# Optimization experiments

Measured on AMD Instinct MI355X. Metric: run time of the kernel, lower is better.

## Reference

```python
import jax, jax.numpy as jnp
import numpy as np

B, N, M = 8, 4096, 2048
IN_DIM, D, CTX_DIM = 512, 512, 768


def setup_inputs() -> dict:
    key = jax.random.key(0)
    k_h, k_hr, k_c, k_a, k_k, k_v, k_o = jax.random.split(key, 7)
    s = 0.02  # init scale for weights
    return {
        "h": jax.random.normal(k_h, (B, N, IN_DIM), dtype=jnp.float32),
        "h_retrieved": jax.random.normal(k_hr, (B, M, CTX_DIM), dtype=jnp.float32),
        # torch nn.Linear convention: weight is [out_features, in_features]
        "W_cond": jax.random.normal(k_c, (IN_DIM, CTX_DIM), dtype=jnp.float32) * s,
        "W_attn": jax.random.normal(k_a, (D, IN_DIM), dtype=jnp.float32) * s,
        "W_k": jax.random.normal(k_k, (D, IN_DIM), dtype=jnp.float32) * s,
        "W_v": jax.random.normal(k_v, (D, IN_DIM), dtype=jnp.float32) * s,
        "W_out": jax.random.normal(k_o, (IN_DIM, D), dtype=jnp.float32) * s,
    }


def reference(h, h_retrieved, W_cond, W_attn, W_k, W_v, W_out):
    # cond_flag is True since context_dim != in_dim
    hr = h_retrieved @ W_cond.T                      # [B, M, in_dim]
    attn = jax.nn.softmax(h @ W_attn.T, axis=-1)     # [B, N, d], softmax over channel dim
    kv_in = jnp.concatenate([h, hr], axis=1)         # [B, N+M, in_dim]
    k = kv_in @ W_k.T                                # [B, N+M, d]
    v = kv_in @ W_v.T                                # [B, N+M, d]
    f = jnp.einsum('bnd,bne->bde', k, v)             # K^T V: [B, d, d]
    h_aug = jnp.einsum('bnd,bde->bne', attn, f)      # [B, N, d]
    return h + h_aug @ W_out.T                       # [B, N, in_dim]
```

## Files before the change

### kernel.cpp

```cpp
#include <hip/hip_runtime.h>
#include <hip/hip_bf16.h>


typedef unsigned short u16;
typedef __bf16 bf16x8 __attribute__((ext_vector_type(8)));
typedef float  f32x4  __attribute__((ext_vector_type(4)));
typedef float  f32v4  __attribute__((ext_vector_type(4)));
typedef u16    u16v4  __attribute__((ext_vector_type(4)));
typedef u16    u16v8  __attribute__((ext_vector_type(8)));

__device__ __forceinline__ u16 f2bf(float f) {
  unsigned u = __builtin_bit_cast(unsigned, f);
  u = u + 0x7FFFu + ((u >> 16) & 1u);
  return (u16)(u >> 16);
}
__device__ __forceinline__ float bf2f(u16 s) {
  return __builtin_bit_cast(float, (unsigned)s << 16);
}

__global__ __launch_bounds__(256) void cvt_dual(const float* __restrict__ src,
                                                u16* __restrict__ dstN,
                                                u16* __restrict__ dstT,
                                                long src_bs, long dstT_bs) {
  __shared__ u16 tile[64][72];
  long bz = blockIdx.z;
  const float* S = src + bz * src_bs;
  u16* DN = dstN + bz * src_bs;
  u16* DT = dstT + bz * dstT_bs;
  int r0 = blockIdx.x * 64;
  int c0 = blockIdx.y * 64;
  int t  = threadIdx.x;
  int tr = t >> 2;
  int tc = (t & 3) * 16;
  const float* sp = &S[(long)(r0 + tr) * 512 + c0 + tc];
#pragma unroll
  for (int q = 0; q < 2; ++q) {
    f32v4 a = *(const f32v4*)(sp + q * 8);
    f32v4 b = *(const f32v4*)(sp + q * 8 + 4);
    u16v8 o;
    o[0] = f2bf(a[0]); o[1] = f2bf(a[1]); o[2] = f2bf(a[2]); o[3] = f2bf(a[3]);
    o[4] = f2bf(b[0]); o[5] = f2bf(b[1]); o[6] = f2bf(b[2]); o[7] = f2bf(b[3]);
    *(u16v8*)&DN[(long)(r0 + tr) * 512 + c0 + tc + q * 8] = o;
    *(u16v8*)&tile[tr][tc + q * 8] = o;
  }
  __syncthreads();
  int tr2 = t >> 3;
  int tc2 = (t & 7) * 8;
#pragma unroll
  for (int it = 0; it < 2; ++it) {
    int cr = it * 32 + tr2;
    u16v8 o;
#pragma unroll
    for (int j = 0; j < 8; ++j) o[j] = tile[tc2 + j][cr];
    *(u16v8*)&DT[(long)(c0 + cr) * 6144 + r0 + tc2] = o;
  }
}

__global__ __launch_bounds__(256) void prep_weights(
    const float* __restrict__ Wc, const float* __restrict__ Wa,
    const float* __restrict__ Wk, const float* __restrict__ Wv,
    const float* __restrict__ Wo,
    u16* __restrict__ wc, u16* __restrict__ wa, u16* __restrict__ wk,
    u16* __restrict__ wv, u16* __restrict__ wvT, u16* __restrict__ wo) {
  __shared__ u16 tile[64][72];
  int bx = blockIdx.x;
  int t = threadIdx.x;
  if (bx < 576) {
    const float* src; u16* dst; long base;
    if (bx < 192)      { src = Wc; dst = wc; base = (long)bx * 2048; }
    else if (bx < 320) { src = Wa; dst = wa; base = (long)(bx - 192) * 2048; }
    else if (bx < 448) { src = Wk; dst = wk; base = (long)(bx - 320) * 2048; }
    else               { src = Wo; dst = wo; base = (long)(bx - 448) * 2048; }
    long i = base + (long)t * 8;
    f32v4 a = *(const f32v4*)(src + i);
    f32v4 b = *(const f32v4*)(src + i + 4);
    u16v8 o;
    o[0] = f2bf(a[0]); o[1] = f2bf(a[1]); o[2] = f2bf(a[2]); o[3] = f2bf(a[3]);
    o[4] = f2bf(b[0]); o[5] = f2bf(b[1]); o[6] = f2bf(b[2]); o[7] = f2bf(b[3]);
    *(u16v8*)(dst + i) = o;
  } else {
    int b2 = bx - 576;
    int r0 = (b2 >> 3) * 64, c0 = (b2 & 7) * 64;
    int tr = t >> 2, tc = (t & 3) * 16;
    const float* sp = &Wv[(long)(r0 + tr) * 512 + c0 + tc];
#pragma unroll
    for (int q = 0; q < 2; ++q) {
      f32v4 a = *(const f32v4*)(sp + q * 8);
      f32v4 b = *(const f32v4*)(sp + q * 8 + 4);
      u16v8 o;
      o[0] = f2bf(a[0]); o[1] = f2bf(a[1]); o[2] = f2bf(a[2]); o[3] = f2bf(a[3]);
      o[4] = f2bf(b[0]); o[5] = f2bf(b[1]); o[6] = f2bf(b[2]); o[7] = f2bf(b[3]);
      *(u16v8*)&wv[(long)(r0 + tr) * 512 + c0 + tc + q * 8] = o;
      *(u16v8*)&tile[tr][tc + q * 8] = o;
    }
    __syncthreads();
    int tr2 = t >> 3, tc2 = (t & 7) * 8;
#pragma unroll
    for (int it = 0; it < 2; ++it) {
      int cr = it * 32 + tr2;
      u16v8 o;
#pragma unroll
      for (int j = 0; j < 8; ++j) o[j] = tile[tc2 + j][cr];
      *(u16v8*)&wvT[(long)(c0 + cr) * 512 + r0 + tc2] = o;
    }
  }
}

__global__ __launch_bounds__(256) void reduce8_bf16(const u16* __restrict__ parts,
                                                    u16* __restrict__ out) {
  long i = (((long)blockIdx.x * 256) + threadIdx.x) * 8;
  long b = i >> 18;
  long r = i & 262143;
  const u16* p = parts + b * 2097152 + r;
  float acc[8] = {};
#pragma unroll
  for (int s = 0; s < 8; ++s) {
    u16v8 v = *(const u16v8*)(p + (long)s * 262144);
#pragma unroll
    for (int j = 0; j < 8; ++j) acc[j] += bf2f(v[j]);
  }
  u16v8 o;
#pragma unroll
  for (int j = 0; j < 8; ++j) o[j] = f2bf(acc[j]);
  *(u16v8*)(out + i) = o;
}

template <int MODE>
__global__ __launch_bounds__(256) void gemm_nt(
    const u16* __restrict__ A, const u16* __restrict__ B, void* __restrict__ Cout,
    const float* __restrict__ Res, int K, int lda, int ldb, int ldc,
    long sA, long sB, long sC, long sS, long sRes, int kslices) {
  __shared__ __align__(16) char smem_c[32768];
  u16* As = (u16*)smem_c;
  u16* Bs = (u16*)(smem_c + 16384);

  int gx = gridDim.x, gy = gridDim.y;
  int nwg = gx * gy * (int)gridDim.z;
  int flat = blockIdx.x + gx * (blockIdx.y + gy * blockIdx.z);
  if ((nwg & 7) == 0) { int q = nwg >> 3; flat = (flat & 7) * q + (flat >> 3); }
  int bx = flat % gx; int tmp = flat / gx; int by = tmp % gy; int z = tmp / gy;

  int b = z / kslices;
  int s = z - b * kslices;
  const u16* Ag = A + (long)b * sA + (long)s * K;
  const u16* Bg = B + (long)b * sB + (long)s * K;

  long m0 = (long)bx * 128;
  long n0 = (long)by * 128;

  int tid  = threadIdx.x;
  int lane = tid & 63;
  int wid  = tid >> 6;
  int wm = wid >> 1, wn = wid & 1;

  int srow = wid * 8 + (lane >> 3);
  int scol = (lane & 7) * 8;

  f32x4 acc[4][4] = {};

  for (int k0 = 0; k0 < K; k0 += 64) {
#pragma unroll
    for (int c = 0; c < 4; ++c) {
      int row = c * 32 + srow;
      __builtin_amdgcn_global_load_lds(
          (const __attribute__((address_space(1))) void*)(Ag + (m0 + row) * lda + k0 + scol),
          (__attribute__((address_space(3))) void*)(As + (c * 32 + wid * 8) * 64),
          16, 0, 0);
    }
#pragma unroll
    for (int c = 0; c < 4; ++c) {
      int row = c * 32 + srow;
      __builtin_amdgcn_global_load_lds(
          (const __attribute__((address_space(1))) void*)(Bg + (n0 + row) * ldb + k0 + scol),
          (__attribute__((address_space(3))) void*)(Bs + (c * 32 + wid * 8) * 64),
          16, 0, 0);
    }
    __syncthreads();
#pragma unroll
    for (int kk = 0; kk < 2; ++kk) {
      int kofs = kk * 32 + (lane >> 4) * 8;
      bf16x8 af[4], bfr[4];
#pragma unroll
      for (int i = 0; i < 4; ++i) {
        af[i]  = *(const bf16x8*)&As[(wm * 64 + i * 16 + (lane & 15)) * 64 + kofs];
        bfr[i] = *(const bf16x8*)&Bs[(wn * 64 + i * 16 + (lane & 15)) * 64 + kofs];
      }
#pragma unroll
      for (int i = 0; i < 4; ++i)
#pragma unroll
        for (int j = 0; j < 4; ++j)
          acc[i][j] = __builtin_amdgcn_mfma_f32_16x16x32_bf16(af[i], bfr[j], acc[i][j], 0, 0, 0);
    }
    __syncthreads();
  }

  float* ep = (float*)(smem_c + wid * 4608);
  long cb  = (long)b * sC + (long)s * sS;
  int row0 = (int)m0 + wm * 64;
  int colb = (int)n0 + wn * 64;
  int lq = lane >> 4;
  int lr = lane & 15;

#pragma unroll
  for (int i = 0; i < 4; ++i) {
#pragma unroll
    for (int j = 0; j < 4; ++j)
#pragma unroll
      for (int r = 0; r < 4; ++r)
        ep[(lq * 4 + r) * 72 + lr + j * 16] = acc[i][j][r];
#pragma unroll
    for (int p = 0; p < 4; ++p) {
      int rl = p * 4 + lq;
      f32x4 v = *(f32x4*)&ep[rl * 72 + lr * 4];
      long off = (long)(row0 + i * 16 + rl) * ldc + colb + lr * 4;
      if (MODE == 0) {
        u16v4 o;
#pragma unroll
        for (int t = 0; t < 4; ++t) o[t] = f2bf(v[t]);
        *(u16v4*)((u16*)Cout + cb + off) = o;
      } else {
        const float* R = Res + (long)b * sRes;
        f32v4 rv = *(const f32v4*)&R[off];
        f32v4 ov;
#pragma unroll
        for (int t = 0; t < 4; ++t) ov[t] = v[t] + rv[t];
        *(f32v4*)((float*)Cout + cb + off) = ov;
      }
    }
  }
}

template <int MODE, bool AF32>
__global__ __launch_bounds__(256) void gemm64(
    const void* __restrict__ Ap, const u16* __restrict__ B, void* __restrict__ Cout,
    const float* __restrict__ Res, int K, int lda, int ldb, int ldc,
    long sA, long sB, long sC, long sRes) {
  __shared__ __align__(16) char smem_c[24576];
  u16* As = (u16*)smem_c;
  u16* Bs = (u16*)(smem_c + 8192);

  int gx = gridDim.x, gy = gridDim.y;
  int nwg = gx * gy * (int)gridDim.z;
  int flat = blockIdx.x + gx * (blockIdx.y + gy * blockIdx.z);
  if ((nwg & 7) == 0) { int q = nwg >> 3; flat = (flat & 7) * q + (flat >> 3); }
  int bx = flat % gx; int tmp = flat / gx; int by = tmp % gy; int b = tmp / gy;

  long n0 = (long)bx * 128;
  long m0 = (long)by * 64;
  const u16* Ag = (const u16*)Ap + (long)b * sA;
  const float* Af = (const float*)Ap + (long)b * sA;
  const u16* Bg = B + (long)b * sB;

  int tid  = threadIdx.x;
  int lane = tid & 63;
  int wid  = tid >> 6;
  int wm = wid >> 1, wn = wid & 1;

  int srow = wid * 8 + (lane >> 3);
  int scol = (lane & 7) * 8;

  f32x4 acc[2][4] = {};

  for (int k0 = 0; k0 < K; k0 += 64) {
    if constexpr (AF32) {
      int arow = tid >> 2;
      int acol = (tid & 3) * 16;
      const float* sp = Af + (m0 + arow) * (long)lda + k0 + acol;
      f32v4 x0 = *(const f32v4*)sp;
      f32v4 x1 = *(const f32v4*)(sp + 4);
      f32v4 x2 = *(const f32v4*)(sp + 8);
      f32v4 x3 = *(const f32v4*)(sp + 12);
      u16v8 o0, o1;
      o0[0] = f2bf(x0[0]); o0[1] = f2bf(x0[1]); o0[2] = f2bf(x0[2]); o0[3] = f2bf(x0[3]);
      o0[4] = f2bf(x1[0]); o0[5] = f2bf(x1[1]); o0[6] = f2bf(x1[2]); o0[7] = f2bf(x1[3]);
      o1[0] = f2bf(x2[0]); o1[1] = f2bf(x2[1]); o1[2] = f2bf(x2[2]); o1[3] = f2bf(x2[3]);
      o1[4] = f2bf(x3[0]); o1[5] = f2bf(x3[1]); o1[6] = f2bf(x3[2]); o1[7] = f2bf(x3[3]);
      *(u16v8*)&As[arow * 64 + acol] = o0;
      *(u16v8*)&As[arow * 64 + acol + 8] = o1;
    } else {
#pragma unroll
      for (int c = 0; c < 2; ++c) {
        int row = c * 32 + srow;
        __builtin_amdgcn_global_load_lds(
            (const __attribute__((address_space(1))) void*)(Ag + (m0 + row) * lda + k0 + scol),
            (__attribute__((address_space(3))) void*)(As + (c * 32 + wid * 8) * 64),
            16, 0, 0);
      }
    }
#pragma unroll
    for (int c = 0; c < 4; ++c) {
      int row = c * 32 + srow;
      __builtin_amdgcn_global_load_lds(
          (const __attribute__((address_space(1))) void*)(Bg + (n0 + row) * ldb + k0 + scol),
          (__attribute__((address_space(3))) void*)(Bs + (c * 32 + wid * 8) * 64),
          16, 0, 0);
    }
    __syncthreads();
#pragma unroll
    for (int kk = 0; kk < 2; ++kk) {
      int kofs = kk * 32 + (lane >> 4) * 8;
      bf16x8 af[2], bfr[4];
#pragma unroll
      for (int i = 0; i < 2; ++i)
        af[i]  = *(const bf16x8*)&As[(wm * 32 + i * 16 + (lane & 15)) * 64 + kofs];
#pragma unroll
      for (int j = 0; j < 4; ++j)
        bfr[j] = *(const bf16x8*)&Bs[(wn * 64 + j * 16 + (lane & 15)) * 64 + kofs];
#pragma unroll
      for (int i = 0; i < 2; ++i)
#pragma unroll
        for (int j = 0; j < 4; ++j)
          acc[i][j] = __builtin_amdgcn_mfma_f32_16x16x32_bf16(af[i], bfr[j], acc[i][j], 0, 0, 0);
    }
    __syncthreads();
  }

  int lq = lane >> 4;
  int lr = lane & 15;

  if (MODE == 0 || MODE == 1) {
    float* ep = (float*)(smem_c + wid * 4608);
    long cb  = (long)b * sC;
    int row0 = (int)m0 + wm * 32;
    int colb = (int)n0 + wn * 64;
#pragma unroll
    for (int i = 0; i < 2; ++i) {
#pragma unroll
      for (int j = 0; j < 4; ++j)
#pragma unroll
        for (int r = 0; r < 4; ++r)
          ep[(lq * 4 + r) * 72 + lr + j * 16] = acc[i][j][r];
#pragma unroll
      for (int p = 0; p < 4; ++p) {
        int rl = p * 4 + lq;
        f32x4 v = *(f32x4*)&ep[rl * 72 + lr * 4];
        long off = (long)(row0 + i * 16 + rl) * ldc + colb + lr * 4;
        if (MODE == 0) {
          u16v4 o;
#pragma unroll
          for (int t = 0; t < 4; ++t) o[t] = f2bf(v[t]);
          *(u16v4*)((u16*)Cout + cb + off) = o;
        } else {
          const float* R = Res + (long)b * sRes;
          f32v4 rv = *(const f32v4*)&R[off];
          f32v4 ov;
#pragma unroll
          for (int t = 0; t < 4; ++t) ov[t] = v[t] + rv[t];
          *(f32v4*)((float*)Cout + cb + off) = ov;
        }
      }
    }
  } else {
    u16* tT = (u16*)smem_c;
#pragma unroll
    for (int i = 0; i < 2; ++i)
#pragma unroll
      for (int j = 0; j < 4; ++j)
#pragma unroll
        for (int r = 0; r < 4; ++r)
          tT[(wn * 64 + j * 16 + lr) * 72 + wm * 32 + i * 16 + lq * 4 + r] = f2bf(acc[i][j][r]);
    __syncthreads();
    long cb = (long)b * sC;
    int ct  = tid >> 1;
    int seg = (tid & 1) * 32;
    u16* dst = (u16*)Cout + cb + (long)(n0 + ct) * ldc + m0 + seg;
    const u16* srcl = &tT[ct * 72 + seg];
#pragma unroll
    for (int q = 0; q < 4; ++q)
      *(u16v8*)(dst + q * 8) = *(const u16v8*)(srcl + q * 8);
  }
}

__global__ __launch_bounds__(256, 2) void gemm_sm(
    const u16* __restrict__ A,
    const u16* __restrict__ Bw,
    u16* __restrict__ C) {
  __shared__ __align__(16) char smem[73728];
  u16* As = (u16*)smem;
  u16* Bs = (u16*)(smem + 8192);

  int nwg = gridDim.x;
  int flat = blockIdx.x;
  if ((nwg & 7) == 0) { int q = nwg >> 3; flat = (flat & 7) * q + (flat >> 3); }
  long m0 = (long)flat * 64;

  int tid = threadIdx.x;
  int lane = tid & 63;
  int wid = tid >> 6;

  int srow = wid * 8 + (lane >> 3);
  int scol = (lane & 7) * 8;

  f32x4 acc[4][8] = {};

  for (int k0 = 0; k0 < 512; k0 += 64) {
#pragma unroll
    for (int c = 0; c < 2; ++c) {
      int row = c * 32 + srow;
      __builtin_amdgcn_global_load_lds(
          (const __attribute__((address_space(1))) void*)(A + (m0 + row) * 512 + k0 + scol),
          (__attribute__((address_space(3))) void*)(As + (c * 32 + wid * 8) * 64),
          16, 0, 0);
    }
#pragma unroll
    for (int c = 0; c < 16; ++c) {
      int row = c * 32 + srow;
      __builtin_amdgcn_global_load_lds(
          (const __attribute__((address_space(1))) void*)(Bw + (long)row * 512 + k0 + scol),
          (__attribute__((address_space(3))) void*)(Bs + (c * 32 + wid * 8) * 64),
          16, 0, 0);
    }
    __syncthreads();
#pragma unroll
    for (int kk = 0; kk < 2; ++kk) {
      int kofs = kk * 32 + (lane >> 4) * 8;
      bf16x8 af[4], bfr[8];
#pragma unroll
      for (int i = 0; i < 4; ++i)
        af[i] = *(const bf16x8*)&As[(i * 16 + (lane & 15)) * 64 + kofs];
#pragma unroll
      for (int j = 0; j < 8; ++j)
        bfr[j] = *(const bf16x8*)&Bs[(wid * 128 + j * 16 + (lane & 15)) * 64 + kofs];
#pragma unroll
      for (int i = 0; i < 4; ++i)
#pragma unroll
        for (int j = 0; j < 8; ++j)
          acc[i][j] = __builtin_amdgcn_mfma_f32_16x16x32_bf16(af[i], bfr[j], acc[i][j], 0, 0, 0);
    }
    __syncthreads();
  }

  int lq = lane >> 4, lr = lane & 15;
  float* sm = (float*)smem;
  float* ss = (float*)(smem + 1024);

#pragma unroll
  for (int i = 0; i < 4; ++i)
#pragma unroll
    for (int r = 0; r < 4; ++r) {
      float m = acc[i][0][r];
#pragma unroll
      for (int j = 1; j < 8; ++j) m = fmaxf(m, acc[i][j][r]);
#pragma unroll
      for (int o = 1; o < 16; o <<= 1) m = fmaxf(m, __shfl_xor(m, o, 16));
      if (lr == 0) sm[(i * 16 + lq * 4 + r) * 4 + wid] = m;
    }
  __syncthreads();
  float rinv[4][4];
#pragma unroll
  for (int i = 0; i < 4; ++i)
#pragma unroll
    for (int r = 0; r < 4; ++r) {
      f32v4 g4 = *(const f32v4*)&sm[(i * 16 + lq * 4 + r) * 4];
      float gm = fmaxf(fmaxf(g4[0], g4[1]), fmaxf(g4[2], g4[3]));
      float s = 0.f;
#pragma unroll
      for (int j = 0; j < 8; ++j) {
        float e = __expf(acc[i][j][r] - gm);
        acc[i][j][r] = e;
        s += e;
      }
#pragma unroll
      for (int o = 1; o < 16; o <<= 1) s += __shfl_xor(s, o, 16);
      if (lr == 0) ss[(i * 16 + lq * 4 + r) * 4 + wid] = s;
    }
  __syncthreads();
#pragma unroll
  for (int i = 0; i < 4; ++i)
#pragma unroll
    for (int r = 0; r < 4; ++r) {
      f32v4 g4 = *(const f32v4*)&ss[(i * 16 + lq * 4 + r) * 4];
      rinv[i][r] = 1.0f / (g4[0] + g4[1] + g4[2] + g4[3]);
    }
  __syncthreads();

  float* ep = (float*)(smem + wid * 4608);
#pragma unroll
  for (int i = 0; i < 4; ++i) {
#pragma unroll
    for (int jh = 0; jh < 2; ++jh) {
#pragma unroll
      for (int j = 0; j < 4; ++j)
#pragma unroll
        for (int r = 0; r < 4; ++r)
          ep[(lq * 4 + r) * 72 + lr + j * 16] = acc[i][jh * 4 + j][r] * rinv[i][r];
#pragma unroll
      for (int p = 0; p < 4; ++p) {
        int rl = p * 4 + lq;
        f32x4 v = *(f32x4*)&ep[rl * 72 + lr * 4];
        u16v4 o;
#pragma unroll
        for (int t = 0; t < 4; ++t) o[t] = f2bf(v[t]);
        *(u16v4*)&C[(m0 + i * 16 + rl) * 512 + wid * 128 + jh * 64 + lr * 4] = o;
      }
    }
  }
}

extern "C" void kernel_launch(void* const* d_in, const int* in_sizes, int n_in,
                              void* d_out, int out_size, void* d_ws, size_t ws_size,
                              hipStream_t stream) {
  (void)in_sizes; (void)n_in; (void)out_size; (void)ws_size;
  const float* h    = (const float*)d_in[0];
  const float* hret = (const float*)d_in[1];
  const float* Wc   = (const float*)d_in[2];
  const float* Wa   = (const float*)d_in[3];
  const float* Wk   = (const float*)d_in[4];
  const float* Wv   = (const float*)d_in[5];
  const float* Wo   = (const float*)d_in[6];
  float* out = (float*)d_out;
  char*  ws  = (char*)d_ws;

  constexpr long MB = 1024 * 1024;
  u16*   w_cond = (u16*)(ws + 0);
  u16*   w_attn = (u16*)(ws + 786432);
  u16*   w_k    = (u16*)(ws + 1310720);
  u16*   w_v    = (u16*)(ws + 1835008);
  u16*   w_out  = (u16*)(ws + 2359296);
  u16*   w_vT   = (u16*)(ws + 2883584);
  u16*   h_bf   = (u16*)(ws + 4 * MB);
  u16*   gparts = (u16*)(ws + 4 * MB);
  u16*   attn   = (u16*)(ws + 36 * MB);
  u16*   g_bf   = (u16*)(ws + 68 * MB);
  u16*   u_mat  = (u16*)(ws + 72 * MB);
  u16*   v1     = (u16*)(ws + 73 * MB);
  u16*   f2t    = (u16*)(ws + 77 * MB);
  u16*   xt     = (u16*)(ws + 84 * MB);

  cvt_dual<<<dim3(64, 8, 8), 256, 0, stream>>>(h, h_bf, xt, 2097152L, 3145728L);
  prep_weights<<<640, 256, 0, stream>>>(Wc, Wa, Wk, Wv, Wo,
      w_cond, w_attn, w_k, w_v, w_vT, w_out);

  gemm64<3, true><<<dim3(4, 32, 8), 256, 0, stream>>>(hret, w_cond, xt + 4096, nullptr,
      768, 768, 768, 6144, 1572864L, 0, 3145728L, 0);

  gemm_sm<<<512, 256, 0, stream>>>(h_bf, w_attn, attn);

  gemm_nt<0><<<dim3(4, 4, 64), 256, 0, stream>>>(xt, xt, gparts, nullptr,
      768, 6144, 6144, 512, 3145728L, 3145728L, 2097152L, 262144L, 0, 8);
  reduce8_bf16<<<1024, 256, 0, stream>>>(gparts, g_bf);

  gemm64<0, false><<<dim3(4, 8, 1), 256, 0, stream>>>(w_out, w_vT, u_mat, nullptr,
      512, 512, 512, 512, 0, 0, 0, 0);
  gemm64<0, false><<<dim3(4, 8, 8), 256, 0, stream>>>(u_mat, g_bf, v1, nullptr,
      512, 512, 512, 512, 0, 262144L, 262144L, 0);
  gemm64<0, false><<<dim3(4, 8, 8), 256, 0, stream>>>(v1, w_k, f2t, nullptr,
      512, 512, 512, 512, 262144L, 0, 262144L, 0);

  gemm64<1, false><<<dim3(4, 64, 8), 256, 0, stream>>>(attn, f2t, out, h,
      512, 512, 512, 512, 2097152L, 262144L, 2097152L, 2097152L);
}
```

Before: 226.5 us.

## Double-buffer LDS tiles in both GEMM kernels to overlap loads with MFMA

Both GEMM kernels now use two LDS buffers per operand and issue the next K-tile's global-to-LDS loads (or fp32 register loads followed by bf16 conversion for the AF32 path) before running the MFMAs on the current tile. This drops one __syncthreads per iteration and is meant to hide global memory latency behind compute. In exchange, LDS use doubles (64KB and 48KB per block), which can lower occupancy, and register pressure rises on the AF32 path. Correctness depends on the s_waitcnt the compiler emits for global_load_lds before the single barrier.

Result: faster. 217.4 us (-4.0%).

```diff
diff --git a/kernel.cpp b/kernel.cpp
--- a/kernel.cpp
+++ b/kernel.cpp
@@ -130,9 +130,7 @@
     const u16* __restrict__ A, const u16* __restrict__ B, void* __restrict__ Cout,
     const float* __restrict__ Res, int K, int lda, int ldb, int ldc,
     long sA, long sB, long sC, long sS, long sRes, int kslices) {
-  __shared__ __align__(16) char smem_c[32768];
-  u16* As = (u16*)smem_c;
-  u16* Bs = (u16*)(smem_c + 16384);
+  __shared__ __align__(16) char smem_c[65536];
 
   int gx = gridDim.x, gy = gridDim.y;
   int nwg = gx * gy * (int)gridDim.z;
@@ -156,34 +154,51 @@
   int srow = wid * 8 + (lane >> 3);
   int scol = (lane & 7) * 8;
 
-  f32x4 acc[4][4] = {};
-
-  for (int k0 = 0; k0 < K; k0 += 64) {
+  auto stageA = [&](u16* Asd, int k0) {
 #pragma unroll
     for (int c = 0; c < 4; ++c) {
       int row = c * 32 + srow;
       __builtin_amdgcn_global_load_lds(
           (const __attribute__((address_space(1))) void*)(Ag + (m0 + row) * lda + k0 + scol),
-          (__attribute__((address_space(3))) void*)(As + (c * 32 + wid * 8) * 64),
+          (__attribute__((address_space(3))) void*)(Asd + (c * 32 + wid * 8) * 64),
           16, 0, 0);
     }
+  };
+  auto stageB = [&](u16* Bsd, int k0) {
 #pragma unroll
     for (int c = 0; c < 4; ++c) {
       int row = c * 32 + srow;
       __builtin_amdgcn_global_load_lds(
           (const __attribute__((address_space(1))) void*)(Bg + (n0 + row) * ldb + k0 + scol),
-          (__attribute__((address_space(3))) void*)(Bs + (c * 32 + wid * 8) * 64),
+          (__attribute__((address_space(3))) void*)(Bsd + (c * 32 + wid * 8) * 64),
           16, 0, 0);
     }
-    __syncthreads();
+  };
+
+  f32x4 acc[4][4] = {};
+  int nk = K >> 6;
+
+  stageA((u16*)smem_c, 0);
+  stageB((u16*)(smem_c + 32768), 0);
+  __syncthreads();
+
+  for (int t = 0; t < nk; ++t) {
+    u16* Asc = (u16*)(smem_c + (t & 1) * 16384);
+    u16* Bsc = (u16*)(smem_c + 32768 + (t & 1) * 16384);
+    if (t + 1 < nk) {
+      u16* Asn = (u16*)(smem_c + ((t + 1) & 1) * 16384);
+      u16* Bsn = (u16*)(smem_c + 32768 + ((t + 1) & 1) * 16384);
+      stageA(Asn, (t + 1) * 64);
+      stageB(Bsn, (t + 1) * 64);
+    }
 #pragma unroll
     for (int kk = 0; kk < 2; ++kk) {
       int kofs = kk * 32 + (lane >> 4) * 8;
       bf16x8 af[4], bfr[4];
 #pragma unroll
       for (int i = 0; i < 4; ++i) {
-        af[i]  = *(const bf16x8*)&As[(wm * 64 + i * 16 + (lane & 15)) * 64 + kofs];
-        bfr[i] = *(const bf16x8*)&Bs[(wn * 64 + i * 16 + (lane & 15)) * 64 + kofs];
+        af[i]  = *(const bf16x8*)&Asc[(wm * 64 + i * 16 + (lane & 15)) * 64 + kofs];
+        bfr[i] = *(const bf16x8*)&Bsc[(wn * 64 + i * 16 + (lane & 15)) * 64 + kofs];
       }
 #pragma unroll
       for (int i = 0; i < 4; ++i)
@@ -216,14 +231,14 @@
       if (MODE == 0) {
         u16v4 o;
 #pragma unroll
-        for (int t = 0; t < 4; ++t) o[t] = f2bf(v[t]);
+        for (int t2 = 0; t2 < 4; ++t2) o[t2] = f2bf(v[t2]);
         *(u16v4*)((u16*)Cout + cb + off) = o;
       } else {
         const float* R = Res + (long)b * sRes;
         f32v4 rv = *(const f32v4*)&R[off];
         f32v4 ov;
 #pragma unroll
-        for (int t = 0; t < 4; ++t) ov[t] = v[t] + rv[t];
+        for (int t2 = 0; t2 < 4; ++t2) ov[t2] = v[t2] + rv[t2];
         *(f32v4*)((float*)Cout + cb + off) = ov;
       }
     }
@@ -235,9 +250,7 @@
     const void* __restrict__ Ap, const u16* __restrict__ B, void* __restrict__ Cout,
     const float* __restrict__ Res, int K, int lda, int ldb, int ldc,
     long sA, long sB, long sC, long sRes) {
-  __shared__ __align__(16) char smem_c[24576];
-  u16* As = (u16*)smem_c;
-  u16* Bs = (u16*)(smem_c + 8192);
+  __shared__ __align__(16) char smem_c[49152];
 
   int gx = gridDim.x, gy = gridDim.y;
   int nwg = gx * gy * (int)gridDim.z;
@@ -258,59 +271,93 @@
 
   int srow = wid * 8 + (lane >> 3);
   int scol = (lane & 7) * 8;
-
-  f32x4 acc[2][4] = {};
-
-  for (int k0 = 0; k0 < K; k0 += 64) {
-    if constexpr (AF32) {
-      int arow = tid >> 2;
-      int acol = (tid & 3) * 16;
-      const float* sp = Af + (m0 + arow) * (long)lda + k0 + acol;
-      f32v4 x0 = *(const f32v4*)sp;
-      f32v4 x1 = *(const f32v4*)(sp + 4);
-      f32v4 x2 = *(const f32v4*)(sp + 8);
-      f32v4 x3 = *(const f32v4*)(sp + 12);
-      u16v8 o0, o1;
-      o0[0] = f2bf(x0[0]); o0[1] = f2bf(x0[1]); o0[2] = f2bf(x0[2]); o0[3] = f2bf(x0[3]);
-      o0[4] = f2bf(x1[0]); o0[5] = f2bf(x1[1]); o0[6] = f2bf(x1[2]); o0[7] = f2bf(x1[3]);
-      o1[0] = f2bf(x2[0]); o1[1] = f2bf(x2[1]); o1[2] = f2bf(x2[2]); o1[3] = f2bf(x2[3]);
-      o1[4] = f2bf(x3[0]); o1[5] = f2bf(x3[1]); o1[6] = f2bf(x3[2]); o1[7] = f2bf(x3[3]);
-      *(u16v8*)&As[arow * 64 + acol] = o0;
-      *(u16v8*)&As[arow * 64 + acol + 8] = o1;
-    } else {
-#pragma unroll
-      for (int c = 0; c < 2; ++c) {
-        int row = c * 32 + srow;
-        __builtin_amdgcn_global_load_lds(
-            (const __attribute__((address_space(1))) void*)(Ag + (m0 + row) * lda + k0 + scol),
-            (__attribute__((address_space(3))) void*)(As + (c * 32 + wid * 8) * 64),
-            16, 0, 0);
-      }
-    }
+  int arow = tid >> 2;
+  int acol = (tid & 3) * 16;
+
+  auto stageA = [&](u16* Asd, int k0) {
+#pragma unroll
+    for (int c = 0; c < 2; ++c) {
+      int row = c * 32 + srow;
+      __builtin_amdgcn_global_load_lds(
+          (const __attribute__((address_space(1))) void*)(Ag + (m0 + row) * lda + k0 + scol),
+          (__attribute__((address_space(3))) void*)(Asd + (c * 32 + wid * 8) * 64),
+          16, 0, 0);
+    }
+  };
+  auto stageB = [&](u16* Bsd, int k0) {
 #pragma unroll
     for (int c = 0; c < 4; ++c) {
       int row = c * 32 + srow;
       __builtin_amdgcn_global_load_lds(
           (const __attribute__((address_space(1))) void*)(Bg + (n0 + row) * ldb + k0 + scol),
-          (__attribute__((address_space(3))) void*)(Bs + (c * 32 + wid * 8) * 64),
+          (__attribute__((address_space(3))) void*)(Bsd + (c * 32 + wid * 8) * 64),
           16, 0, 0);
     }
-    __syncthreads();
+  };
+  auto cvtA = [&](u16* Asd, const f32v4& x0, const f32v4& x1,
+                  const f32v4& x2, const f32v4& x3) {
+    u16v8 o0, o1;
+    o0[0] = f2bf(x0[0]); o0[1] = f2bf(x0[1]); o0[2] = f2bf(x0[2]); o0[3] = f2bf(x0[3]);
+    o0[4] = f2bf(x1[0]); o0[5] = f2bf(x1[1]); o0[6] = f2bf(x1[2]); o0[7] = f2bf(x1[3]);
+    o1[0] = f2bf(x2[0]); o1[1] = f2bf(x2[1]); o1[2] = f2bf(x2[2]); o1[3] = f2bf(x2[3]);
+    o1[4] = f2bf(x3[0]); o1[5] = f2bf(x3[1]); o1[6] = f2bf(x3[2]); o1[7] = f2bf(x3[3]);
+    *(u16v8*)&Asd[arow * 64 + acol] = o0;
+    *(u16v8*)&Asd[arow * 64 + acol + 8] = o1;
+  };
+
+  f32x4 acc[2][4] = {};
+  int nk = K >> 6;
+
+  if constexpr (AF32) {
+    const float* sp = Af + (m0 + arow) * (long)lda + acol;
+    f32v4 x0 = *(const f32v4*)sp;
+    f32v4 x1 = *(const f32v4*)(sp + 4);
+    f32v4 x2 = *(const f32v4*)(sp + 8);
+    f32v4 x3 = *(const f32v4*)(sp + 12);
+    cvtA((u16*)smem_c, x0, x1, x2, x3);
+  } else {
+    stageA((u16*)smem_c, 0);
+  }
+  stageB((u16*)(smem_c + 16384), 0);
+  __syncthreads();
+
+  for (int t = 0; t < nk; ++t) {
+    u16* Asc = (u16*)(smem_c + (t & 1) * 8192);
+    u16* Bsc = (u16*)(smem_c + 16384 + (t & 1) * 16384);
+    u16* Asn = (u16*)(smem_c + ((t + 1) & 1) * 8192);
+    u16* Bsn = (u16*)(smem_c + 16384 + ((t + 1) & 1) * 16384);
+    bool more = (t + 1) < nk;
+    f32v4 x0, x1, x2, x3;
+    if (more) {
+      if constexpr (AF32) {
+        const float* sp = Af + (m0 + arow) * (long)lda + (t + 1) * 64 + acol;
+        x0 = *(const f32v4*)sp;
+        x1 = *(const f32v4*)(sp + 4);
+        x2 = *(const f32v4*)(sp + 8);
+        x3 = *(const f32v4*)(sp + 12);
+      } else {
+        stageA(Asn, (t + 1) * 64);
+      }
+      stageB(Bsn, (t + 1) * 64);
+    }
 #pragma unroll
     for (int kk = 0; kk < 2; ++kk) {
       int kofs = kk * 32 + (lane >> 4) * 8;
       bf16x8 af[2], bfr[4];
 #pragma unroll
       for (int i = 0; i < 2; ++i)
-        af[i]  = *(const bf16x8*)&As[(wm * 32 + i * 16 + (lane & 15)) * 64 + kofs];
+        af[i]  = *(const bf16x8*)&Asc[(wm * 32 + i * 16 + (lane & 15)) * 64 + kofs];
 #pragma unroll
       for (int j = 0; j < 4; ++j)
-        bfr[j] = *(const bf16x8*)&Bs[(wn * 64 + j * 16 + (lane & 15)) * 64 + kofs];
+        bfr[j] = *(const bf16x8*)&Bsc[(wn * 64 + j * 16 + (lane & 15)) * 64 + kofs];
 #pragma unroll
       for (int i = 0; i < 2; ++i)
 #pragma unroll
         for (int j = 0; j < 4; ++j)
           acc[i][j] = __builtin_amdgcn_mfma_f32_16x16x32_bf16(af[i], bfr[j], acc[i][j], 0, 0, 0);
+    }
+    if constexpr (AF32) {
+      if (more) cvtA(Asn, x0, x1, x2, x3);
     }
     __syncthreads();
   }
@@ -338,14 +385,14 @@
         if (MODE == 0) {
           u16v4 o;
 #pragma unroll
-          for (int t = 0; t < 4; ++t) o[t] = f2bf(v[t]);
+          for (int t2 = 0; t2 < 4; ++t2) o[t2] = f2bf(v[t2]);
           *(u16v4*)((u16*)Cout + cb + off) = o;
         } else {
           const float* R = Res + (long)b * sRes;
           f32v4 rv = *(const f32v4*)&R[off];
           f32v4 ov;
 #pragma unroll
-          for (int t = 0; t < 4; ++t) ov[t] = v[t] + rv[t];
+          for (int t2 = 0; t2 < 4; ++t2) ov[t2] = v[t2] + rv[t2];
           *(f32v4*)((float*)Cout + cb + off) = ov;
         }
       }
```
